# Kernel tuning notes

Measured on AMD Instinct MI355X. Metric: run time of the kernel, lower is better.

The kernel has to match this reference:

```python
import jax, jax.numpy as jnp
import numpy as np

DIM = 96
NUM_HEADS = 3
WIN = 7  # window_size (square)


def _relative_position_index(wh, ww):
    coords = np.stack(np.meshgrid(np.arange(wh), np.arange(ww), indexing='ij'))  # [2, wh, ww]
    flat = coords.reshape(2, -1)  # [2, n]
    rel = flat[:, :, None] - flat[:, None, :]  # [2, n, n]
    rel = rel.transpose(1, 2, 0).astype(np.int64)
    rel[..., 0] += wh - 1
    rel[..., 1] += ww - 1
    rel[..., 0] *= 2 * ww - 1
    return rel.sum(-1)  # [n, n]


def setup_inputs() -> dict:
    key = jax.random.key(0)
    ks = jax.random.split(key, 9)
    b, n, c = 8192, WIN * WIN, DIM
    std = 0.02
    inp = {
        'x': jax.random.normal(ks[0], (b, n, c), jnp.float32),
        'v': jax.random.normal(ks[1], (b, n, c), jnp.float32),
        'w_q': jax.random.normal(ks[2], (c, c), jnp.float32) * std,
        'b_q': jnp.zeros((c,), jnp.float32),
        'w_kv': jax.random.normal(ks[3], (c, 2 * c), jnp.float32) * std,
        'b_kv': jnp.zeros((2 * c,), jnp.float32),
        'w_proj': jax.random.normal(ks[4], (c, c), jnp.float32) * std,
        'b_proj': jnp.zeros((c,), jnp.float32),
        'rpb_table': jax.random.normal(ks[5], ((2 * WIN - 1) * (2 * WIN - 1), NUM_HEADS), jnp.float32) * std,
        'rel_index': jnp.asarray(_relative_position_index(WIN, WIN), jnp.int32),
    }
    return inp


def reference(x, v, w_q, b_q, w_kv, b_kv, w_proj, b_proj, rpb_table, rel_index):
    b, n, c = x.shape
    h = NUM_HEADS
    hd = c // h
    scale = hd ** -0.5
    # q: [b, h, n, hd]
    q = (x @ w_q + b_q).reshape(b, n, h, hd).transpose(0, 2, 1, 3) * scale
    kv = (v @ w_kv + b_kv).reshape(b, n, 2, h, hd)
    k = kv[:, :, 0].transpose(0, 2, 1, 3)  # [b, h, n, hd]
    vv = kv[:, :, 1].transpose(0, 2, 1, 3)
    attn = jnp.einsum('bhqd,bhkd->bhqk', q, k)  # [b, h, n, n]
    bias = rpb_table[rel_index.reshape(-1)].reshape(n, n, h).transpose(2, 0, 1)  # [h, n, n]
    attn = jax.nn.softmax(attn + bias[None], axis=-1)
    out = jnp.einsum('bhqk,bhkd->bhqd', attn, vv).transpose(0, 2, 1, 3).reshape(b, n, c)
    return out @ w_proj + b_proj
```

## Files before the change

kernel.cpp:

```cpp
#include <hip/hip_runtime.h>
#include <hip/hip_bf16.h>

typedef __bf16 bf16x8 __attribute__((ext_vector_type(8)));
typedef float f32x4 __attribute__((ext_vector_type(4)));
typedef short s16x8 __attribute__((ext_vector_type(8)));
typedef short s16x4 __attribute__((ext_vector_type(4)));

#define NTOK 49
#define CDIM 96
#define KS_S 104
#define VT_S 72
#define BN_S 104

__device__ __forceinline__ unsigned short f2bf(float f) {
  __hip_bfloat16 h = __float2bfloat16(f);
  return __builtin_bit_cast(unsigned short, h);
}

__device__ __forceinline__ bf16x8 ld_cvt8(const float* p) {
  float4 a = *(const float4*)p;
  float4 b = *(const float4*)(p + 4);
  s16x8 r;
  r[0] = (short)f2bf(a.x); r[1] = (short)f2bf(a.y);
  r[2] = (short)f2bf(a.z); r[3] = (short)f2bf(a.w);
  r[4] = (short)f2bf(b.x); r[5] = (short)f2bf(b.y);
  r[6] = (short)f2bf(b.z); r[7] = (short)f2bf(b.w);
  return __builtin_bit_cast(bf16x8, r);
}

__global__ void prep(const float* __restrict__ wq, const float* __restrict__ wkv,
                     const float* __restrict__ wproj, const float* __restrict__ rpb,
                     const int* __restrict__ relidx, unsigned short* __restrict__ wsT,
                     float* __restrict__ biasf) {
  const int total = 36864 + 3 * 49 * 64;
  for (int i = blockIdx.x * 256 + threadIdx.x; i < total; i += gridDim.x * 256) {
    if (i < 9216) {
      int oc = i / 96, ic = i - oc * 96;
      wsT[i] = f2bf(wq[ic * 96 + oc]);
    } else if (i < 27648) {
      int j = i - 9216; int oc = j / 96, ic = j - oc * 96;
      wsT[i] = f2bf(wkv[ic * 192 + oc]);
    } else if (i < 36864) {
      int j = i - 27648; int oc = j / 96, ic = j - oc * 96;
      wsT[i] = f2bf(wproj[ic * 96 + oc]);
    } else {
      int j = i - 36864; int h = j / 3136; int rc = j - h * 3136;
      int r = rc >> 6, c = rc & 63;
      biasf[j] = (c < 49) ? rpb[relidx[r * 49 + c] * 3 + h] : 0.f;
    }
  }
}

__launch_bounds__(256, 4)
__global__ void attn_fused(const float* __restrict__ xg, const float* __restrict__ vg,
                           const float* __restrict__ bq, const float* __restrict__ bkv,
                           const float* __restrict__ bproj,
                           const unsigned short* __restrict__ wsT,
                           const float* __restrict__ biasf,
                           float* __restrict__ outg) {
  __shared__ __align__(16) unsigned char smem[37328];
  unsigned short* Ks  = (unsigned short*)smem;
  unsigned short* VVT = (unsigned short*)(smem + 10192);

  const int tid = threadIdx.x;
  const int lane = tid & 63;
  const int wv = tid >> 6;
  const int c16 = lane & 15;
  const int g4 = lane >> 4;
  const int win = blockIdx.x;
  const int q0 = (wv == 0) ? 0 : (wv == 1) ? 16 : (wv == 2) ? 32 : 33;
  unsigned short* bnc = (unsigned short*)(smem + 24016) + wv * (16 * BN_S);

  const float* xrow = xg + (size_t)win * (NTOK * CDIM) + (q0 + c16) * CDIM;
  const float* vrow = vg + (size_t)win * (NTOK * CDIM) + (q0 + c16) * CDIM;

  bf16x8 xf[3];
#pragma unroll
  for (int k = 0; k < 3; ++k) xf[k] = ld_cvt8(xrow + k * 32 + g4 * 8);
  const float scale = 0.17677669529663687f;
#pragma unroll
  for (int nt = 0; nt < 6; ++nt) {
    f32x4 acc = {0, 0, 0, 0};
    const int ocl = nt * 16 + c16;
#pragma unroll
    for (int k = 0; k < 3; ++k) {
      bf16x8 b = *(const bf16x8*)(wsT + ocl * 96 + k * 32 + g4 * 8);
      acc = __builtin_amdgcn_mfma_f32_16x16x32_bf16(xf[k], b, acc, 0, 0, 0);
    }
    float bias = bq[ocl];
#pragma unroll
    for (int r = 0; r < 4; ++r)
      bnc[(4 * g4 + r) * BN_S + ocl] = f2bf((acc[r] + bias) * scale);
  }

  bf16x8 vf[3];
#pragma unroll
  for (int k = 0; k < 3; ++k) vf[k] = ld_cvt8(vrow + k * 32 + g4 * 8);
#pragma unroll
  for (int nt = 0; nt < 12; ++nt) {
    f32x4 acc = {0, 0, 0, 0};
    const int ocl = nt * 16 + c16;
#pragma unroll
    for (int k = 0; k < 3; ++k) {
      bf16x8 b = *(const bf16x8*)(wsT + 9216 + ocl * 96 + k * 32 + g4 * 8);
      acc = __builtin_amdgcn_mfma_f32_16x16x32_bf16(vf[k], b, acc, 0, 0, 0);
    }
    float bias = bkv[ocl];
    if (nt < 6) {
#pragma unroll
      for (int r = 0; r < 4; ++r)
        Ks[(q0 + 4 * g4 + r) * KS_S + ocl] = f2bf(acc[r] + bias);
    } else {
      int dim = ocl - 96;
      int rb = q0 + 4 * g4;
      if (wv < 3) {
        s16x4 p;
#pragma unroll
        for (int r = 0; r < 4; ++r) p[r] = (short)f2bf(acc[r] + bias);
        *(s16x4*)(VVT + dim * VT_S + rb) = p;
      } else {
#pragma unroll
        for (int r = 0; r < 4; ++r)
          VVT[dim * VT_S + rb + r] = f2bf(acc[r] + bias);
      }
    }
  }
  __syncthreads();

  bf16x8 qf[3];
#pragma unroll
  for (int h = 0; h < 3; ++h)
    qf[h] = *(const bf16x8*)(bnc + c16 * BN_S + h * 32 + g4 * 8);

  s16x8 vmask;
#pragma unroll
  for (int j = 0; j < 8; ++j)
    vmask[j] = (short)(((32 + g4 * 8 + j) < 49) ? 0xFFFF : 0x0000);

  f32x4 oacc[6] = {{0,0,0,0},{0,0,0,0},{0,0,0,0},{0,0,0,0},{0,0,0,0},{0,0,0,0}};

  for (int h = 0; h < 3; ++h) {
    f32x4 s[4];
#pragma unroll
    for (int kt = 0; kt < 4; ++kt) {
      bf16x8 ak = *(const bf16x8*)(Ks + (16 * kt + c16) * KS_S + h * 32 + g4 * 8);
      s[kt] = __builtin_amdgcn_mfma_f32_16x16x32_bf16(ak, qf[h], (f32x4){0,0,0,0}, 0, 0, 0);
    }
    const int q = q0 + c16;
    const float* brow = biasf + (h * 49 + q) * 64 + 4 * g4;
    float vals[16];
    float mx = -1e30f;
#pragma unroll
    for (int kt = 0; kt < 4; ++kt) {
      f32x4 bv = *(const f32x4*)(brow + 16 * kt);
#pragma unroll
      for (int r = 0; r < 4; ++r) {
        int key = 16 * kt + 4 * g4 + r;
        float vl = (kt < 3 || key < 49) ? (s[kt][r] + bv[r]) : -1e30f;
        vals[kt * 4 + r] = vl;
        mx = fmaxf(mx, vl);
      }
    }
    mx = fmaxf(mx, __shfl_xor(mx, 16, 64));
    mx = fmaxf(mx, __shfl_xor(mx, 32, 64));
    float sum = 0.f;
#pragma unroll
    for (int j = 0; j < 16; ++j) { vals[j] = __expf(vals[j] - mx); sum += vals[j]; }
    sum += __shfl_xor(sum, 16, 64);
    sum += __shfl_xor(sum, 32, 64);
    float rinv = 1.0f / sum;
#pragma unroll
    for (int kt = 0; kt < 4; ++kt) {
      s16x4 p;
#pragma unroll
      for (int r = 0; r < 4; ++r) p[r] = (short)f2bf(vals[kt * 4 + r] * rinv);
      *(s16x4*)(bnc + c16 * BN_S + 16 * kt + 4 * g4) = p;
    }
    asm volatile("s_waitcnt lgkmcnt(0)" ::: "memory");
    __builtin_amdgcn_sched_barrier(0);
    bf16x8 ap0 = *(const bf16x8*)(bnc + c16 * BN_S + g4 * 8);
    bf16x8 ap1 = *(const bf16x8*)(bnc + c16 * BN_S + 32 + g4 * 8);
#pragma unroll
    for (int dt = 0; dt < 2; ++dt) {
      int dim = h * 32 + dt * 16 + c16;
      bf16x8 bv0 = *(const bf16x8*)(VVT + dim * VT_S + g4 * 8);
      s16x8 b1 = *(const s16x8*)(VVT + dim * VT_S + 32 + g4 * 8);
      b1 &= vmask;
      f32x4 o = __builtin_amdgcn_mfma_f32_16x16x32_bf16(ap0, bv0, (f32x4){0,0,0,0}, 0, 0, 0);
      o = __builtin_amdgcn_mfma_f32_16x16x32_bf16(ap1, __builtin_bit_cast(bf16x8, b1), o, 0, 0, 0);
#pragma unroll
      for (int r = 0; r < 4; ++r)
        bnc[(4 * g4 + r) * BN_S + dt * 16 + c16] = f2bf(o[r]);
    }
    asm volatile("s_waitcnt lgkmcnt(0)" ::: "memory");
    __builtin_amdgcn_sched_barrier(0);
    bf16x8 bo = *(const bf16x8*)(bnc + c16 * BN_S + g4 * 8);
#pragma unroll
    for (int mt = 0; mt < 6; ++mt) {
      bf16x8 a = *(const bf16x8*)(wsT + 27648 + (mt * 16 + c16) * 96 + h * 32 + g4 * 8);
      oacc[mt] = __builtin_amdgcn_mfma_f32_16x16x32_bf16(a, bo, oacc[mt], 0, 0, 0);
    }
    asm volatile("s_waitcnt lgkmcnt(0)" ::: "memory");
    __builtin_amdgcn_sched_barrier(0);
  }

  {
    const bool store_ok = (wv < 3) || (c16 == 15);
    const int token = q0 + c16;
    float* orow = outg + (size_t)win * (NTOK * CDIM) + token * 96;
#pragma unroll
    for (int mt = 0; mt < 6; ++mt) {
      int oc0 = mt * 16 + g4 * 4;
      if (store_ok) {
        float4 bb = *(const float4*)(bproj + oc0);
        float4 o4;
        o4.x = oacc[mt][0] + bb.x; o4.y = oacc[mt][1] + bb.y;
        o4.z = oacc[mt][2] + bb.z; o4.w = oacc[mt][3] + bb.w;
        *(float4*)(orow + oc0) = o4;
      }
    }
  }
}

extern "C" void kernel_launch(void* const* d_in, const int* in_sizes, int n_in,
                              void* d_out, int out_size, void* d_ws, size_t ws_size,
                              hipStream_t stream) {
  const float* x     = (const float*)d_in[0];
  const float* v     = (const float*)d_in[1];
  const float* wq    = (const float*)d_in[2];
  const float* bq    = (const float*)d_in[3];
  const float* wkv   = (const float*)d_in[4];
  const float* bkv   = (const float*)d_in[5];
  const float* wproj = (const float*)d_in[6];
  const float* bproj = (const float*)d_in[7];
  const float* rpb   = (const float*)d_in[8];
  const int*   relidx= (const int*)d_in[9];
  float* out = (float*)d_out;
  unsigned short* wsT = (unsigned short*)d_ws;
  float* biasf = (float*)((char*)d_ws + 73728);
  int nwin = in_sizes[0] / (NTOK * CDIM);

  hipLaunchKernelGGL(prep, dim3(181), dim3(256), 0, stream,
                     wq, wkv, wproj, rpb, relidx, wsT, biasf);
  hipLaunchKernelGGL(attn_fused, dim3(nwin), dim3(256), 0, stream,
                     x, v, bq, bkv, bproj, wsT, biasf, out);
}
```

Before: 258.7 us.

## Software-pipeline per-head attention stages and split K/V projection across waves

```diff
diff --git a/kernel.cpp b/kernel.cpp
--- a/kernel.cpp
+++ b/kernel.cpp
@@ -9,8 +9,18 @@
 #define NTOK 49
 #define CDIM 96
 #define KS_S 104
-#define VT_S 72
-#define BN_S 104
+#define VT_S 56
+#define BN_S 136
+#define LOG2E 1.4426950408889634f
+
+#if __has_builtin(__builtin_amdgcn_exp2f)
+#define EXP2F(x) __builtin_amdgcn_exp2f(x)
+#else
+#define EXP2F(x) exp2f(x)
+#endif
+
+#define DRAIN() do { asm volatile("s_waitcnt lgkmcnt(0)" ::: "memory"); \
+                     __builtin_amdgcn_sched_barrier(0); } while (0)
 
 __device__ __forceinline__ unsigned short f2bf(float f) {
   __hip_bfloat16 h = __float2bfloat16(f);
@@ -46,7 +56,7 @@
     } else {
       int j = i - 36864; int h = j / 3136; int rc = j - h * 3136;
       int r = rc >> 6, c = rc & 63;
-      biasf[j] = (c < 49) ? rpb[relidx[r * 49 + c] * 3 + h] : 0.f;
+      biasf[j] = (c < 49) ? rpb[relidx[r * 49 + c] * 3 + h] * LOG2E : 0.f;
     }
   }
 }
@@ -58,7 +68,7 @@
                            const unsigned short* __restrict__ wsT,
                            const float* __restrict__ biasf,
                            float* __restrict__ outg) {
-  __shared__ __align__(16) unsigned char smem[37328];
+  __shared__ __align__(16) unsigned char smem[38352];
   unsigned short* Ks  = (unsigned short*)smem;
   unsigned short* VVT = (unsigned short*)(smem + 10192);
 
@@ -69,15 +79,28 @@
   const int g4 = lane >> 4;
   const int win = blockIdx.x;
   const int q0 = (wv == 0) ? 0 : (wv == 1) ? 16 : (wv == 2) ? 32 : 33;
-  unsigned short* bnc = (unsigned short*)(smem + 24016) + wv * (16 * BN_S);
-
-  const float* xrow = xg + (size_t)win * (NTOK * CDIM) + (q0 + c16) * CDIM;
-  const float* vrow = vg + (size_t)win * (NTOK * CDIM) + (q0 + c16) * CDIM;
-
-  bf16x8 xf[3];
-#pragma unroll
-  for (int k = 0; k < 3; ++k) xf[k] = ld_cvt8(xrow + k * 32 + g4 * 8);
-  const float scale = 0.17677669529663687f;
+  unsigned short* bnc = (unsigned short*)(smem + 20944) + wv * (16 * BN_S);
+
+  const int mp = wv & 1;
+  const bool isK = (wv < 2);
+  const int m0 = mp ? 32 : 0;
+  const int m1 = mp ? 33 : 16;
+
+  const float* base = xg + (size_t)win * (NTOK * CDIM);
+  const float* vbase = vg + (size_t)win * (NTOK * CDIM);
+  const float* xrow = base + (q0 + c16) * CDIM;
+  const float* vrow0 = vbase + (m0 + c16) * CDIM;
+  const float* vrow1 = vbase + (m1 + c16) * CDIM;
+
+  bf16x8 xf[3], vf0[3], vf1[3];
+#pragma unroll
+  for (int k = 0; k < 3; ++k) {
+    xf[k]  = ld_cvt8(xrow  + k * 32 + g4 * 8);
+    vf0[k] = ld_cvt8(vrow0 + k * 32 + g4 * 8);
+    vf1[k] = ld_cvt8(vrow1 + k * 32 + g4 * 8);
+  }
+
+  const float scale = 0.2550348742f;
 #pragma unroll
   for (int nt = 0; nt < 6; ++nt) {
     f32x4 acc = {0, 0, 0, 0};
@@ -93,44 +116,45 @@
       bnc[(4 * g4 + r) * BN_S + ocl] = f2bf((acc[r] + bias) * scale);
   }
 
-  bf16x8 vf[3];
-#pragma unroll
-  for (int k = 0; k < 3; ++k) vf[k] = ld_cvt8(vrow + k * 32 + g4 * 8);
-#pragma unroll
-  for (int nt = 0; nt < 12; ++nt) {
-    f32x4 acc = {0, 0, 0, 0};
-    const int ocl = nt * 16 + c16;
+#pragma unroll
+  for (int nt = 0; nt < 6; ++nt) {
+    const int ocl = (isK ? 0 : 96) + nt * 16 + c16;
+    f32x4 a0 = {0, 0, 0, 0}, a1 = {0, 0, 0, 0};
 #pragma unroll
     for (int k = 0; k < 3; ++k) {
       bf16x8 b = *(const bf16x8*)(wsT + 9216 + ocl * 96 + k * 32 + g4 * 8);
-      acc = __builtin_amdgcn_mfma_f32_16x16x32_bf16(vf[k], b, acc, 0, 0, 0);
+      a0 = __builtin_amdgcn_mfma_f32_16x16x32_bf16(vf0[k], b, a0, 0, 0, 0);
+      a1 = __builtin_amdgcn_mfma_f32_16x16x32_bf16(vf1[k], b, a1, 0, 0, 0);
     }
     float bias = bkv[ocl];
-    if (nt < 6) {
+    if (isK) {
 #pragma unroll
       for (int r = 0; r < 4; ++r)
-        Ks[(q0 + 4 * g4 + r) * KS_S + ocl] = f2bf(acc[r] + bias);
+        Ks[(m0 + 4 * g4 + r) * KS_S + ocl] = f2bf(a0[r] + bias);
+#pragma unroll
+      for (int r = 0; r < 4; ++r)
+        Ks[(m1 + 4 * g4 + r) * KS_S + ocl] = f2bf(a1[r] + bias);
     } else {
       int dim = ocl - 96;
-      int rb = q0 + 4 * g4;
-      if (wv < 3) {
-        s16x4 p;
-#pragma unroll
-        for (int r = 0; r < 4; ++r) p[r] = (short)f2bf(acc[r] + bias);
-        *(s16x4*)(VVT + dim * VT_S + rb) = p;
+      s16x4 p0;
+#pragma unroll
+      for (int r = 0; r < 4; ++r) p0[r] = (short)f2bf(a0[r] + bias);
+      *(s16x4*)(VVT + dim * VT_S + (m0 + 4 * g4)) = p0;
+      if (mp == 0) {
+        s16x4 p1;
+#pragma unroll
+        for (int r = 0; r < 4; ++r) p1[r] = (short)f2bf(a1[r] + bias);
+        *(s16x4*)(VVT + dim * VT_S + (16 + 4 * g4)) = p1;
       } else {
 #pragma unroll
         for (int r = 0; r < 4; ++r)
-          VVT[dim * VT_S + rb + r] = f2bf(acc[r] + bias);
+          VVT[dim * VT_S + 33 + 4 * g4 + r] = f2bf(a1[r] + bias);
       }
     }
   }
   __syncthreads();
 
-  bf16x8 qf[3];
-#pragma unroll
-  for (int h = 0; h < 3; ++h)
-    qf[h] = *(const bf16x8*)(bnc + c16 * BN_S + h * 32 + g4 * 8);
+  const int q = q0 + c16;
 
   s16x8 vmask;
 #pragma unroll
@@ -139,33 +163,31 @@
 
   f32x4 oacc[6] = {{0,0,0,0},{0,0,0,0},{0,0,0,0},{0,0,0,0},{0,0,0,0},{0,0,0,0}};
 
-  for (int h = 0; h < 3; ++h) {
-    f32x4 s[4];
-#pragma unroll
-    for (int kt = 0; kt < 4; ++kt) {
-      bf16x8 ak = *(const bf16x8*)(Ks + (16 * kt + c16) * KS_S + h * 32 + g4 * 8);
-      s[kt] = __builtin_amdgcn_mfma_f32_16x16x32_bf16(ak, qf[h], (f32x4){0,0,0,0}, 0, 0, 0);
-    }
-    const int q = q0 + c16;
-    const float* brow = biasf + (h * 49 + q) * 64 + 4 * g4;
+  auto softmax_pw = [&](const f32x4* s, const f32x4* bv, int pcol) {
     float vals[16];
-    float mx = -1e30f;
-#pragma unroll
-    for (int kt = 0; kt < 4; ++kt) {
-      f32x4 bv = *(const f32x4*)(brow + 16 * kt);
+#pragma unroll
+    for (int kt = 0; kt < 4; ++kt)
 #pragma unroll
       for (int r = 0; r < 4; ++r) {
         int key = 16 * kt + 4 * g4 + r;
-        float vl = (kt < 3 || key < 49) ? (s[kt][r] + bv[r]) : -1e30f;
-        vals[kt * 4 + r] = vl;
-        mx = fmaxf(mx, vl);
+        vals[kt * 4 + r] = (kt < 3 || key < 49) ? (s[kt][r] + bv[kt][r]) : -1e30f;
       }
-    }
+    float m8[8];
+#pragma unroll
+    for (int j = 0; j < 8; ++j) m8[j] = fmaxf(vals[j], vals[j + 8]);
+    float ma = fmaxf(m8[0], m8[4]), mb = fmaxf(m8[1], m8[5]);
+    float mc = fmaxf(m8[2], m8[6]), md = fmaxf(m8[3], m8[7]);
+    float mx = fmaxf(fmaxf(ma, mb), fmaxf(mc, md));
     mx = fmaxf(mx, __shfl_xor(mx, 16, 64));
     mx = fmaxf(mx, __shfl_xor(mx, 32, 64));
-    float sum = 0.f;
-#pragma unroll
-    for (int j = 0; j < 16; ++j) { vals[j] = __expf(vals[j] - mx); sum += vals[j]; }
+    float e[16];
+#pragma unroll
+    for (int j = 0; j < 16; ++j) e[j] = EXP2F(vals[j] - mx);
+    float s8[8];
+#pragma unroll
+    for (int j = 0; j < 8; ++j) s8[j] = e[j] + e[j + 8];
+    float sa = s8[0] + s8[4], sb = s8[1] + s8[5], sc = s8[2] + s8[6], sd = s8[3] + s8[7];
+    float sum = (sa + sb) + (sc + sd);
     sum += __shfl_xor(sum, 16, 64);
     sum += __shfl_xor(sum, 32, 64);
     float rinv = 1.0f / sum;
@@ -173,13 +195,14 @@
     for (int kt = 0; kt < 4; ++kt) {
       s16x4 p;
 #pragma unroll
-      for (int r = 0; r < 4; ++r) p[r] = (short)f2bf(vals[kt * 4 + r] * rinv);
-      *(s16x4*)(bnc + c16 * BN_S + 16 * kt + 4 * g4) = p;
-    }
-    asm volatile("s_waitcnt lgkmcnt(0)" ::: "memory");
-    __builtin_amdgcn_sched_barrier(0);
-    bf16x8 ap0 = *(const bf16x8*)(bnc + c16 * BN_S + g4 * 8);
-    bf16x8 ap1 = *(const bf16x8*)(bnc + c16 * BN_S + 32 + g4 * 8);
+      for (int r = 0; r < 4; ++r) p[r] = (short)f2bf(e[kt * 4 + r] * rinv);
+      *(s16x4*)(bnc + c16 * BN_S + pcol + 16 * kt + 4 * g4) = p;
+    }
+  };
+
+  auto pv_out = [&](int h, int pcol, int ocol) {
+    bf16x8 ap0 = *(const bf16x8*)(bnc + c16 * BN_S + pcol + g4 * 8);
+    bf16x8 ap1 = *(const bf16x8*)(bnc + c16 * BN_S + pcol + 32 + g4 * 8);
 #pragma unroll
     for (int dt = 0; dt < 2; ++dt) {
       int dim = h * 32 + dt * 16 + c16;
@@ -190,24 +213,76 @@
       o = __builtin_amdgcn_mfma_f32_16x16x32_bf16(ap1, __builtin_bit_cast(bf16x8, b1), o, 0, 0, 0);
 #pragma unroll
       for (int r = 0; r < 4; ++r)
-        bnc[(4 * g4 + r) * BN_S + dt * 16 + c16] = f2bf(o[r]);
-    }
-    asm volatile("s_waitcnt lgkmcnt(0)" ::: "memory");
-    __builtin_amdgcn_sched_barrier(0);
-    bf16x8 bo = *(const bf16x8*)(bnc + c16 * BN_S + g4 * 8);
+        bnc[(4 * g4 + r) * BN_S + ocol + dt * 16 + c16] = f2bf(o[r]);
+    }
+  };
+
+  auto oproj = [&](int h, int ocol) {
+    bf16x8 bo = *(const bf16x8*)(bnc + c16 * BN_S + ocol + g4 * 8);
 #pragma unroll
     for (int mt = 0; mt < 6; ++mt) {
       bf16x8 a = *(const bf16x8*)(wsT + 27648 + (mt * 16 + c16) * 96 + h * 32 + g4 * 8);
       oacc[mt] = __builtin_amdgcn_mfma_f32_16x16x32_bf16(a, bo, oacc[mt], 0, 0, 0);
     }
-    asm volatile("s_waitcnt lgkmcnt(0)" ::: "memory");
-    __builtin_amdgcn_sched_barrier(0);
-  }
+  };
+
+  f32x4 b0v[4], b1v[4];
+  {
+    const float* br0 = biasf + q * 64 + 4 * g4;
+    const float* br1 = biasf + (49 + q) * 64 + 4 * g4;
+#pragma unroll
+    for (int kt = 0; kt < 4; ++kt) {
+      b0v[kt] = *(const f32x4*)(br0 + 16 * kt);
+      b1v[kt] = *(const f32x4*)(br1 + 16 * kt);
+    }
+  }
+  bf16x8 qf0 = *(const bf16x8*)(bnc + c16 * BN_S + g4 * 8);
+  bf16x8 qf1 = *(const bf16x8*)(bnc + c16 * BN_S + 32 + g4 * 8);
+  bf16x8 qf2 = *(const bf16x8*)(bnc + c16 * BN_S + 64 + g4 * 8);
+
+  f32x4 s0[4], s1[4];
+#pragma unroll
+  for (int kt = 0; kt < 4; ++kt) {
+    bf16x8 ak = *(const bf16x8*)(Ks + (16 * kt + c16) * KS_S + g4 * 8);
+    s0[kt] = __builtin_amdgcn_mfma_f32_16x16x32_bf16(ak, qf0, (f32x4){0,0,0,0}, 0, 0, 0);
+  }
+#pragma unroll
+  for (int kt = 0; kt < 4; ++kt) {
+    bf16x8 ak = *(const bf16x8*)(Ks + (16 * kt + c16) * KS_S + 32 + g4 * 8);
+    s1[kt] = __builtin_amdgcn_mfma_f32_16x16x32_bf16(ak, qf1, (f32x4){0,0,0,0}, 0, 0, 0);
+  }
+  softmax_pw(s0, b0v, 0);
+  softmax_pw(s1, b1v, 64);
+
+  f32x4 b2v[4];
+  {
+    const float* br2 = biasf + (98 + q) * 64 + 4 * g4;
+#pragma unroll
+    for (int kt = 0; kt < 4; ++kt) b2v[kt] = *(const f32x4*)(br2 + 16 * kt);
+  }
+  f32x4 s2[4];
+#pragma unroll
+  for (int kt = 0; kt < 4; ++kt) {
+    bf16x8 ak = *(const bf16x8*)(Ks + (16 * kt + c16) * KS_S + 64 + g4 * 8);
+    s2[kt] = __builtin_amdgcn_mfma_f32_16x16x32_bf16(ak, qf2, (f32x4){0,0,0,0}, 0, 0, 0);
+  }
+
+  DRAIN();
+  pv_out(0, 0, 0);
+  pv_out(1, 64, 32);
+  softmax_pw(s2, b2v, 64);
+
+  DRAIN();
+  oproj(0, 0);
+  oproj(1, 32);
+  pv_out(2, 64, 96);
+
+  DRAIN();
+  oproj(2, 96);
 
   {
     const bool store_ok = (wv < 3) || (c16 == 15);
-    const int token = q0 + c16;
-    float* orow = outg + (size_t)win * (NTOK * CDIM) + token * 96;
+    float* orow = outg + (size_t)win * (NTOK * CDIM) + q * 96;
 #pragma unroll
     for (int mt = 0; mt < 6; ++mt) {
       int oc0 = mt * 16 + g4 * 4;
```

After: 251.0 us. -3.0%, faster.
